# Optimization experiments

Measured on AMD Instinct MI355X. Metric: run time of the kernel, lower is better.

The kernel has to match this reference:

```python
import jax, jax.numpy as jnp
from jax import lax
import numpy as np

H = 16        # hidden_size == input_size
L = 8         # num_layers


def _lstm_layer(x_seq, Wih, Whh, bih, bhh):
    # x_seq: [B, T, H] -> outputs [B, T, H]; PyTorch gate order i,f,g,o
    B = x_seq.shape[0]
    b = bih + bhh  # [4H]

    def step(carry, xt):
        h, c = carry
        gates = xt @ Wih.T + h @ Whh.T + b  # [B, 4H]
        i, f, g, o = jnp.split(gates, 4, axis=-1)
        c = jax.nn.sigmoid(f) * c + jax.nn.sigmoid(i) * jnp.tanh(g)
        h = jax.nn.sigmoid(o) * jnp.tanh(c)
        return (h, c), h

    h0 = jnp.zeros((B, H), x_seq.dtype)
    (_, _), hs = lax.scan(step, (h0, h0), jnp.swapaxes(x_seq, 0, 1))
    return jnp.swapaxes(hs, 0, 1)  # [B, T, H]


def setup_inputs() -> dict:
    key = jax.random.key(0)
    ks = jax.random.split(key, 9)
    s = 1.0 / np.sqrt(H)  # PyTorch default init scale
    x = jax.random.normal(ks[0], (2048, 512, H), dtype=jnp.float32)
    W_ih = jax.random.uniform(ks[1], (L, 4 * H, H), jnp.float32, -s, s)
    W_hh = jax.random.uniform(ks[2], (L, 4 * H, H), jnp.float32, -s, s)
    b_ih = jax.random.uniform(ks[3], (L, 4 * H), jnp.float32, -s, s)
    b_hh = jax.random.uniform(ks[4], (L, 4 * H), jnp.float32, -s, s)
    Wp = jax.random.uniform(ks[5], (3, H), jnp.float32, -s, s)
    bp = jax.random.uniform(ks[6], (3,), jnp.float32, -s, s)
    Wo = jax.random.uniform(ks[7], (3, H), jnp.float32, -s, s)
    bo = jax.random.uniform(ks[8], (3,), jnp.float32, -s, s)
    return {"x": x, "W_ih": W_ih, "W_hh": W_hh, "b_ih": b_ih, "b_hh": b_hh,
            "Wp": Wp, "bp": bp, "Wo": Wo, "bo": bo}


def reference(x, W_ih, W_hh, b_ih, b_hh, Wp, bp, Wo, bo):
    h = x
    for l in range(L):  # fixed small layer count
        h = _lstm_layer(h, W_ih[l], W_hh[l], b_ih[l], b_hh[l])
    last = h[:, -1, :]                       # [B, H]
    position = last @ Wp.T + bp              # [B, 3]
    orientation = jnp.tanh(last @ Wo.T + bo) # [B, 3]
    return jnp.concatenate((position, orientation), axis=1)  # [B, 6]
```

## Files before the change

### kernel.cpp

```cpp
#include <hip/hip_runtime.h>
#include <math.h>

typedef _Float16 f16x8 __attribute__((ext_vector_type(8)));
typedef float    f32x4 __attribute__((ext_vector_type(4)));

constexpr int kT    = 512;
constexpr int kH    = 16;
constexpr int kL    = 8;
constexpr int kG    = 64;
constexpr int kNB   = 8;
constexpr int kPad  = 24;
constexpr int kRows = 9;
constexpr int kSlots= 16;
constexpr int kLyr  = kL + 1;
constexpr int kSE   = kLyr * kRows * kPad;
constexpr int kIters= 33;

constexpr float kL2E = 1.4426950408889634f;

__device__ __forceinline__ float ex2(float w)  { return __builtin_amdgcn_exp2f(w); }
__device__ __forceinline__ float rcpf(float e) { return __builtin_amdgcn_rcpf(e); }
__device__ __forceinline__ void  cbar()        { asm volatile("" ::: "memory"); }

__global__ __launch_bounds__(1024, 4)
void lstm_bg(const float* __restrict__ x,
             const float* __restrict__ Wih, const float* __restrict__ Whh,
             const float* __restrict__ bih, const float* __restrict__ bhh,
             const float* __restrict__ Wp,  const float* __restrict__ bpos,
             const float* __restrict__ Wo,  const float* __restrict__ bori,
             float* __restrict__ out)
{
    const int tid  = threadIdx.x;
    const int wv   = tid >> 6;
    const int l    = wv & 7;
    const int g    = wv >> 3;
    const int lane = tid & 63;
    const int n    = lane & 15;
    const int q    = lane >> 4;
    const int bl   = n & 3;
    const int br   = 4 * g + bl;
    const int g2   = (n >> 2) & 1;
    const int hi   = n >> 3;
    const bool bact = ((q >> 1) == g2);

    __shared__ __align__(16) _Float16 hb[kSlots][kLyr][kRows][kPad];

    {
        int* hz = (int*)&hb[0][0][0][0];
        for (int i = tid; i < (int)(sizeof(hb) / 4); i += 1024) hz[i] = 0;
    }
    __syncthreads();

    const float asc = ((n & 3) == 2) ? (-2.0f * kL2E) : (-kL2E);
    auto loadA = [&](const float* W, int T) -> f16x8 {
        const int wrow = (n & 3) * 16 + (n >> 2) + 4 * (q >> 1) + 8 * T;
        const float* src = W + (size_t)l * kG * kH + wrow * kH;
        f16x8 a;
        #pragma unroll
        for (int j = 0; j < 8; ++j)
            a[j] = (_Float16)(asc * src[(q & 1) * 8 + j]);
        return a;
    };
    const f16x8 A1T0 = loadA(Wih, 0), A1T1 = loadA(Wih, 1);
    const f16x8 A2T0 = loadA(Whh, 0), A2T1 = loadA(Whh, 1);

    const int u0b = q + 4 * g2;
    f32x4 biasT0, biasT1;
    #pragma unroll
    for (int r = 0; r < 4; ++r) {
        const float sc = (r == 2) ? (-2.0f * kL2E) : (-kL2E);
        const int g0 = l * kG + r * 16 + u0b;
        biasT0[r] = sc * (bih[g0] + bhh[g0]);
        biasT1[r] = sc * (bih[g0 + 8] + bhh[g0 + 8]);
    }

    const int boff = (bact ? br * kPad : 8 * kPad) + (q & 1) * 8;
    const _Float16* b1b = &hb[0][l    ][0][0] + boff;
    const _Float16* b2b = &hb[0][l + 1][0][0] + boff;
    const int um = u0b + 8 * hi;
    _Float16* hw = &hb[0][l + 1][br][um];
    _Float16* xw = &hb[0][0][br][um];

    const float* xg_ptr =
        x + ((size_t)(blockIdx.x * kNB + br) * kT) * kH;
    float xa = 0.f, xb = 0.f, xc = 0.f;
    if (l == 0) {
        #pragma unroll
        for (int t = 0; t < 3; ++t)
            *(xw + ((t + 15) & 15) * kSE) = (_Float16)xg_ptr[t * kH + um];
        xa = xg_ptr[3 * kH + um];
        xb = xg_ptr[4 * kH + um];
        xc = xg_ptr[5 * kH + um];
    }
    __syncthreads();

    const f16x8 B1p = *(const f16x8*)(b1b + 15 * kSE);
    f32x4 dInT0 = __builtin_amdgcn_mfma_f32_16x16x32_f16(A1T0, B1p, biasT0, 0, 0, 0);
    f32x4 dInT1 = __builtin_amdgcn_mfma_f32_16x16x32_f16(A1T1, B1p, biasT1, 0, 0, 0);

    f16x8 B2r;
    #pragma unroll
    for (int j = 0; j < 8; ++j) B2r[j] = (_Float16)0.f;

    float c0 = 0.f;
    const int tl = 2 * l;

    #pragma unroll 1
    for (int it = 0; it < kIters; ++it) {
        const int sb = it * 16;
        #pragma unroll
        for (int k = 0; k < 16; ++k) {
            const int s = sb + k;
            const int slotR = k * kSE;
            const int slotW = ((k + 1) & 15) * kSE;
            const int slotX = ((k + 2) & 15) * kSE;
            const bool active = ((unsigned)(s - tl) < (unsigned)kT);

            const f16x8 B1n = *(const f16x8*)(b1b + slotR);

            f32x4 dT0 = __builtin_amdgcn_mfma_f32_16x16x32_f16(A2T0, B2r, dInT0, 0, 0, 0);
            f32x4 dT1 = __builtin_amdgcn_mfma_f32_16x16x32_f16(A2T1, B2r, dInT1, 0, 0, 0);

            f32x4 d;
            #pragma unroll
            for (int r = 0; r < 4; ++r) d[r] = hi ? dT1[r] : dT0[r];

            const float Ei = ex2(fminf(d[0], 40.0f));
            const float Ef = ex2(fminf(d[1], 40.0f));
            const float Eg = ex2(fminf(d[2], 40.0f));
            const float Eo = ex2(fminf(d[3], 60.0f));
            const float Dg = 1.0f + Eg;
            const float Df = 1.0f + Ef;
            const float P1  = fmaf(Ei, Dg, Dg);
            const float den = Df * P1;
            const float t2  = fmaf(-Eg, Df, Df);
            const float num = fmaf(c0, P1, t2);
            float cn = num * rcpf(den);
            cn = active ? cn : 0.0f;
            c0 = cn;
            const float ac = fminf(cn * (-2.0f * kL2E), 60.0f);
            const float Ec = ex2(ac);
            const float Do = 1.0f + Eo;
            const float R2 = rcpf(fmaf(Do, Ec, Do));
            const float h0 = fmaf(-Ec, R2, R2);

            *(hw + slotW) = (_Float16)h0;

            if (l == 0) {
                *(xw + slotX) = (_Float16)xa;
                xa = xb; xb = xc;
                int tn = s + 6; if (tn > kT - 1) tn = kT - 1;
                xc = xg_ptr[(size_t)tn * kH + um];
            }

            cbar();
            B2r = *(const f16x8*)(b2b + slotW);

            dInT0 = __builtin_amdgcn_mfma_f32_16x16x32_f16(A1T0, B1n, biasT0, 0, 0, 0);
            dInT1 = __builtin_amdgcn_mfma_f32_16x16x32_f16(A1T1, B1n, biasT1, 0, 0, 0);

            asm volatile("s_waitcnt lgkmcnt(1)\n\ts_barrier" ::: "memory");
        }
    }

    __syncthreads();

    if (wv == 15) {
        const int bb = lane >> 3;
        const int r  = lane & 7;
        if (r < 6) {
            const bool  isP   = (r < 3);
            const float* wrow = isP ? (Wp + r * kH) : (Wo + (r - 3) * kH);
            float acc = isP ? bpos[r] : bori[r - 3];
            #pragma unroll
            for (int u = 0; u < kH; ++u)
                acc = fmaf((float)hb[14][kL][bb][u], wrow[u], acc);
            if (!isP) {
                const float Et = ex2(-2.0f * kL2E * acc);
                acc = fmaf(2.0f, rcpf(1.0f + Et), -1.0f);
            }
            out[(size_t)(blockIdx.x * kNB + bb) * 6 + r] = acc;
        }
    }
}

extern "C" void kernel_launch(void* const* d_in, const int* in_sizes, int n_in,
                              void* d_out, int out_size, void* d_ws, size_t ws_size,
                              hipStream_t stream) {
    const float* x    = (const float*)d_in[0];
    const float* Wih  = (const float*)d_in[1];
    const float* Whh  = (const float*)d_in[2];
    const float* bih  = (const float*)d_in[3];
    const float* bhh  = (const float*)d_in[4];
    const float* Wp   = (const float*)d_in[5];
    const float* bpos = (const float*)d_in[6];
    const float* Wo   = (const float*)d_in[7];
    const float* bori = (const float*)d_in[8];
    float* out = (float*)d_out;

    const int B = in_sizes[0] / (kT * kH);
    lstm_bg<<<dim3(B / kNB), dim3(1024), 0, stream>>>(x, Wih, Whh, bih, bhh,
                                                      Wp, bpos, Wo, bori, out);
}
```

Measured before the change: 305.1 us.

## Batch four timesteps per barrier epoch with 4-layer skew and smaller blocks

Switches from one barrier per timestep to one per 4-step epoch. Each layer now lags the one below it by four steps, and an 8-slot double-buffered LDS ring alternates halves between even and odd layers. Blocks shrink to 512 threads with 4 batch rows each, which doubles the grid, and the padding on LDS rows is removed. The goal is to cut barrier count and synchronisation stalls, at the cost of a deeper pipeline fill (more epochs) and possible LDS bank conflicts from the unpadded rows.

After: 303.5 us. About the same (-0.5%).

```diff
diff --git a/kernel.cpp b/kernel.cpp
--- a/kernel.cpp
+++ b/kernel.cpp
@@ -4,26 +4,24 @@
 typedef _Float16 f16x8 __attribute__((ext_vector_type(8)));
 typedef float    f32x4 __attribute__((ext_vector_type(4)));
 
-constexpr int kT    = 512;
-constexpr int kH    = 16;
-constexpr int kL    = 8;
-constexpr int kG    = 64;
-constexpr int kNB   = 8;
-constexpr int kPad  = 24;
-constexpr int kRows = 9;
-constexpr int kSlots= 16;
-constexpr int kLyr  = kL + 1;
-constexpr int kSE   = kLyr * kRows * kPad;
-constexpr int kIters= 33;
+constexpr int kT     = 512;
+constexpr int kH     = 16;
+constexpr int kL     = 8;
+constexpr int kNB    = 4;
+constexpr int kSlots = 8;
+constexpr int kLyr   = kL + 1;
+constexpr int kRows  = 5;
+constexpr int kRowE  = 16;
+constexpr int kSE    = kLyr * kRows * kRowE;
+constexpr int kEpochs= 136;
 
 constexpr float kL2E = 1.4426950408889634f;
 
 __device__ __forceinline__ float ex2(float w)  { return __builtin_amdgcn_exp2f(w); }
 __device__ __forceinline__ float rcpf(float e) { return __builtin_amdgcn_rcpf(e); }
-__device__ __forceinline__ void  cbar()        { asm volatile("" ::: "memory"); }
 
-__global__ __launch_bounds__(1024, 4)
-void lstm_bg(const float* __restrict__ x,
+__global__ __launch_bounds__(512, 4)
+void lstm_e4(const float* __restrict__ x,
              const float* __restrict__ Wih, const float* __restrict__ Whh,
              const float* __restrict__ bih, const float* __restrict__ bhh,
              const float* __restrict__ Wp,  const float* __restrict__ bpos,
@@ -31,30 +29,27 @@
              float* __restrict__ out)
 {
     const int tid  = threadIdx.x;
-    const int wv   = tid >> 6;
-    const int l    = wv & 7;
-    const int g    = wv >> 3;
+    const int l    = tid >> 6;
     const int lane = tid & 63;
     const int n    = lane & 15;
     const int q    = lane >> 4;
     const int bl   = n & 3;
-    const int br   = 4 * g + bl;
     const int g2   = (n >> 2) & 1;
     const int hi   = n >> 3;
     const bool bact = ((q >> 1) == g2);
 
-    __shared__ __align__(16) _Float16 hb[kSlots][kLyr][kRows][kPad];
+    __shared__ __align__(16) _Float16 hb[kSlots][kLyr][kRows][kRowE];
 
     {
         int* hz = (int*)&hb[0][0][0][0];
-        for (int i = tid; i < (int)(sizeof(hb) / 4); i += 1024) hz[i] = 0;
+        for (int i = tid; i < (int)(sizeof(hb) / 4); i += 512) hz[i] = 0;
     }
     __syncthreads();
 
     const float asc = ((n & 3) == 2) ? (-2.0f * kL2E) : (-kL2E);
     auto loadA = [&](const float* W, int T) -> f16x8 {
         const int wrow = (n & 3) * 16 + (n >> 2) + 4 * (q >> 1) + 8 * T;
-        const float* src = W + (size_t)l * kG * kH + wrow * kH;
+        const float* src = W + (size_t)l * 64 * kH + wrow * kH;
         f16x8 a;
         #pragma unroll
         for (int j = 0; j < 8; ++j)
@@ -69,57 +64,54 @@
     #pragma unroll
     for (int r = 0; r < 4; ++r) {
         const float sc = (r == 2) ? (-2.0f * kL2E) : (-kL2E);
-        const int g0 = l * kG + r * 16 + u0b;
+        const int g0 = l * 64 + r * 16 + u0b;
         biasT0[r] = sc * (bih[g0] + bhh[g0]);
         biasT1[r] = sc * (bih[g0 + 8] + bhh[g0 + 8]);
     }
 
-    const int boff = (bact ? br * kPad : 8 * kPad) + (q & 1) * 8;
+    const int boff = (bact ? bl * kRowE : 4 * kRowE) + (q & 1) * 8;
     const _Float16* b1b = &hb[0][l    ][0][0] + boff;
     const _Float16* b2b = &hb[0][l + 1][0][0] + boff;
     const int um = u0b + 8 * hi;
-    _Float16* hw = &hb[0][l + 1][br][um];
-    _Float16* xw = &hb[0][0][br][um];
+    _Float16* hw = &hb[0][l + 1][bl][um];
+    _Float16* xw = &hb[0][0][bl][um];
 
-    const float* xg_ptr =
-        x + ((size_t)(blockIdx.x * kNB + br) * kT) * kH;
-    float xa = 0.f, xb = 0.f, xc = 0.f;
+    const float* xg = x + ((size_t)(blockIdx.x * kNB + bl) * kT) * kH + um;
+    float xr[4] = {0.f, 0.f, 0.f, 0.f};
     if (l == 0) {
         #pragma unroll
-        for (int t = 0; t < 3; ++t)
-            *(xw + ((t + 15) & 15) * kSE) = (_Float16)xg_ptr[t * kH + um];
-        xa = xg_ptr[3 * kH + um];
-        xb = xg_ptr[4 * kH + um];
-        xc = xg_ptr[5 * kH + um];
+        for (int t = 0; t < 8; ++t)
+            hb[t][0][bl][um] = (_Float16)xg[(size_t)t * kH];
+        #pragma unroll
+        for (int j = 0; j < 4; ++j)
+            xr[j] = xg[(size_t)(8 + j) * kH];
     }
-    __syncthreads();
-
-    const f16x8 B1p = *(const f16x8*)(b1b + 15 * kSE);
-    f32x4 dInT0 = __builtin_amdgcn_mfma_f32_16x16x32_f16(A1T0, B1p, biasT0, 0, 0, 0);
-    f32x4 dInT1 = __builtin_amdgcn_mfma_f32_16x16x32_f16(A1T1, B1p, biasT1, 0, 0, 0);
 
     f16x8 B2r;
     #pragma unroll
     for (int j = 0; j < 8; ++j) B2r[j] = (_Float16)0.f;
-
     float c0 = 0.f;
-    const int tl = 2 * l;
+    int te   = -4 * l;
+    int sOfs = (l & 1) ? 4 * kSE : 0;
 
     #pragma unroll 1
-    for (int it = 0; it < kIters; ++it) {
-        const int sb = it * 16;
+    for (int ep = 0; ep < kEpochs; ++ep) {
+        const _Float16* b1p = b1b + sOfs;
+        const _Float16* b2p = b2b + sOfs;
+        _Float16* hwp = hw + sOfs;
+        _Float16* xwp = xw + sOfs;
+
         #pragma unroll
-        for (int k = 0; k < 16; ++k) {
-            const int s = sb + k;
-            const int slotR = k * kSE;
-            const int slotW = ((k + 1) & 15) * kSE;
-            const int slotX = ((k + 2) & 15) * kSE;
-            const bool active = ((unsigned)(s - tl) < (unsigned)kT);
+        for (int j = 0; j < 4; ++j) {
+            const int t = te + j;
+            const bool active = ((unsigned)t < (unsigned)kT);
 
-            const f16x8 B1n = *(const f16x8*)(b1b + slotR);
+            const f16x8 B1 = *(const f16x8*)(b1p + j * kSE);
 
-            f32x4 dT0 = __builtin_amdgcn_mfma_f32_16x16x32_f16(A2T0, B2r, dInT0, 0, 0, 0);
-            f32x4 dT1 = __builtin_amdgcn_mfma_f32_16x16x32_f16(A2T1, B2r, dInT1, 0, 0, 0);
+            f32x4 dInT0 = __builtin_amdgcn_mfma_f32_16x16x32_f16(A1T0, B1, biasT0, 0, 0, 0);
+            f32x4 dInT1 = __builtin_amdgcn_mfma_f32_16x16x32_f16(A1T1, B1, biasT1, 0, 0, 0);
+            f32x4 dT0   = __builtin_amdgcn_mfma_f32_16x16x32_f16(A2T0, B2r, dInT0, 0, 0, 0);
+            f32x4 dT1   = __builtin_amdgcn_mfma_f32_16x16x32_f16(A2T1, B2r, dInT1, 0, 0, 0);
 
             f32x4 d;
             #pragma unroll
@@ -144,28 +136,24 @@
             const float R2 = rcpf(fmaf(Do, Ec, Do));
             const float h0 = fmaf(-Ec, R2, R2);
 
-            *(hw + slotW) = (_Float16)h0;
+            *(hwp + j * kSE) = (_Float16)h0;
+            B2r = *(const f16x8*)(b2p + j * kSE);
 
             if (l == 0) {
-                *(xw + slotX) = (_Float16)xa;
-                xa = xb; xb = xc;
-                int tn = s + 6; if (tn > kT - 1) tn = kT - 1;
-                xc = xg_ptr[(size_t)tn * kH + um];
+                *(xwp + j * kSE) = (_Float16)xr[j];
+                int ti = te + 12 + j; if (ti > kT - 1) ti = kT - 1;
+                xr[j] = xg[(size_t)ti * kH];
             }
+        }
 
-            cbar();
-            B2r = *(const f16x8*)(b2b + slotW);
-
-            dInT0 = __builtin_amdgcn_mfma_f32_16x16x32_f16(A1T0, B1n, biasT0, 0, 0, 0);
-            dInT1 = __builtin_amdgcn_mfma_f32_16x16x32_f16(A1T1, B1n, biasT1, 0, 0, 0);
-
-            asm volatile("s_waitcnt lgkmcnt(1)\n\ts_barrier" ::: "memory");
-        }
+        te += 4;
+        sOfs ^= 4 * kSE;
+        asm volatile("s_waitcnt lgkmcnt(0)\n\ts_barrier" ::: "memory");
     }
 
     __syncthreads();
 
-    if (wv == 15) {
+    if (l == kL - 1 && lane < 32) {
         const int bb = lane >> 3;
         const int r  = lane & 7;
         if (r < 6) {
@@ -174,7 +162,7 @@
             float acc = isP ? bpos[r] : bori[r - 3];
             #pragma unroll
             for (int u = 0; u < kH; ++u)
-                acc = fmaf((float)hb[14][kL][bb][u], wrow[u], acc);
+                acc = fmaf((float)hb[7][kL][bb][u], wrow[u], acc);
             if (!isP) {
                 const float Et = ex2(-2.0f * kL2E * acc);
                 acc = fmaf(2.0f, rcpf(1.0f + Et), -1.0f);
@@ -199,6 +187,6 @@
     float* out = (float*)d_out;
 
     const int B = in_sizes[0] / (kT * kH);
-    lstm_bg<<<dim3(B / kNB), dim3(1024), 0, stream>>>(x, Wih, Whh, bih, bhh,
-                                                      Wp, bpos, Wo, bori, out);
+    lstm_e4<<<dim3(B / kNB), dim3(512), 0, stream>>>(x, Wih, Whh, bih, bhh,
+                                                     Wp, bpos, Wo, bori, out);
 }
```
